# Kernel tuning notes

Measured on AMD Instinct MI355X. Metric: run time of the kernel, lower is better.

The kernel has to match this reference:

```python
import jax, jax.numpy as jnp
import numpy as np

B, N, NODE_DIM, HID_DIM = 64, 4096, 128, 128
D = NODE_DIM + HID_DIM  # concat of ndata['h'] and ndata['x']


def setup_inputs() -> dict:
    key = jax.random.key(0)
    k1, k2, k3, k4 = jax.random.split(key, 4)
    feats = jax.random.normal(k1, (B, N, D), dtype=jnp.float32)
    # per-graph node counts in [1, N] (split_batch asserts size != 0)
    node_counts = jax.random.randint(k2, (B,), 1, N + 1, dtype=jnp.int32)
    Wi = jax.random.normal(k3, (D, 1), dtype=jnp.float32) * 0.05   # project_i weight
    bi = jnp.zeros((1,), dtype=jnp.float32)
    Wj = jax.random.normal(k4, (D, HID_DIM), dtype=jnp.float32) * 0.05  # project_j weight
    bj = jnp.zeros((HID_DIM,), dtype=jnp.float32)
    return {"feats": feats, "node_counts": node_counts,
            "Wi": Wi, "bi": bi, "Wj": Wj, "bj": bj}


def reference(feats, node_counts, Wi, bi, Wj, bj):
    # mask: True at padded node slots (equivalent to zero-pad + sum==0 in split_batch)
    n = feats.shape[1]
    mask = jnp.arange(n)[None, :] >= node_counts[:, None]          # [B, N]
    feats = jnp.where(mask[..., None], 0.0, feats)                  # zero padding rows
    scores = feats @ Wi + bi                                        # [B, N, 1]
    scores = jnp.where(mask[..., None], -100000.0, scores)          # masked_fill
    h1 = jax.nn.softmax(scores, axis=1)                             # softmax over nodes
    h2 = feats @ Wj + bj                                            # [B, N, HID_DIM]
    return jnp.einsum('bni,bnj->bj', h1, h2)                        # [B, HID_DIM]
```

## Files before the change

### kernel.cpp

```cpp
#include <hip/hip_runtime.h>


#define NDIM 256
#define HID 128
#define NMAX 4096
#define ROWS_PER_BLK 160
#define NCHUNK 26
#define PSTRIDE 260
#define FLAG_MAGIC 0x5EED5EEDu

__global__ __launch_bounds__(512) void pool_fused(
    const float* __restrict__ feats, const int* __restrict__ counts,
    const float* __restrict__ Wi, const float* __restrict__ bi,
    const float* __restrict__ Wj, const float* __restrict__ bj,
    unsigned int* __restrict__ flags, float* __restrict__ part_g,
    float* __restrict__ out)
{
    const int b     = blockIdx.y;
    const int count = counts[b];
    const int tid   = threadIdx.x;
    const int nch   = (count + ROWS_PER_BLK - 1) / ROWS_PER_BLK;

    __shared__ float lds_acc[8][NDIM];
    __shared__ float lds_l[8];
    __shared__ float red[2][NDIM];
    __shared__ float redl[2];
    __shared__ float pooled[NDIM];
    __shared__ float tmp[4][HID];

    if (blockIdx.x < NCHUNK) {
        const int row0 = blockIdx.x * ROWS_PER_BLK;
        if (row0 >= count) return;
        const int row_end = min(row0 + ROWS_PER_BLK, count);

        const int lane = tid & 63;
        const int wv   = tid >> 6;
        const int g    = lane >> 4;
        const int q    = lane & 15;

        const float4* Wi4 = reinterpret_cast<const float4*>(Wi);
        const float4 wi0 = Wi4[q], wi1 = Wi4[16 + q], wi2 = Wi4[32 + q], wi3 = Wi4[48 + q];
        const float  fbi = bi[0];

        const float* fb = feats + (size_t)b * NMAX * NDIM;

        float4 a0 = {0,0,0,0}, a1 = {0,0,0,0}, a2 = {0,0,0,0}, a3 = {0,0,0,0};
        float lsum = 0.f;

        const int wbase = row0 + wv * 20;
        #pragma unroll
        for (int it = 0; it < 5; ++it) {
            const int r = wbase + it * 4 + g;
            const bool valid = (r < row_end);
            float4 f0 = {0,0,0,0}, f1 = {0,0,0,0}, f2 = {0,0,0,0}, f3 = {0,0,0,0};
            if (valid) {
                const float4* rp = reinterpret_cast<const float4*>(fb + (size_t)r * NDIM);
                f0 = rp[q]; f1 = rp[16 + q]; f2 = rp[32 + q]; f3 = rp[48 + q];
            }
            float sp = f0.x*wi0.x + f0.y*wi0.y + f0.z*wi0.z + f0.w*wi0.w
                     + f1.x*wi1.x + f1.y*wi1.y + f1.z*wi1.z + f1.w*wi1.w
                     + f2.x*wi2.x + f2.y*wi2.y + f2.z*wi2.z + f2.w*wi2.w
                     + f3.x*wi3.x + f3.y*wi3.y + f3.z*wi3.z + f3.w*wi3.w;
            sp += __shfl_xor(sp, 1, 64);
            sp += __shfl_xor(sp, 2, 64);
            sp += __shfl_xor(sp, 4, 64);
            sp += __shfl_xor(sp, 8, 64);
            const float w = valid ? __expf(sp + fbi) : 0.f;
            lsum += w;
            a0.x += w*f0.x; a0.y += w*f0.y; a0.z += w*f0.z; a0.w += w*f0.w;
            a1.x += w*f1.x; a1.y += w*f1.y; a1.z += w*f1.z; a1.w += w*f1.w;
            a2.x += w*f2.x; a2.y += w*f2.y; a2.z += w*f2.z; a2.w += w*f2.w;
            a3.x += w*f3.x; a3.y += w*f3.y; a3.z += w*f3.z; a3.w += w*f3.w;
        }

        #define COMB(x) x += __shfl_xor(x, 16, 64); x += __shfl_xor(x, 32, 64)
        COMB(a0.x); COMB(a0.y); COMB(a0.z); COMB(a0.w);
        COMB(a1.x); COMB(a1.y); COMB(a1.z); COMB(a1.w);
        COMB(a2.x); COMB(a2.y); COMB(a2.z); COMB(a2.w);
        COMB(a3.x); COMB(a3.y); COMB(a3.z); COMB(a3.w);
        COMB(lsum);
        #undef COMB

        if (g == 0) {
            float* dst = &lds_acc[wv][0];
            *reinterpret_cast<float4*>(&dst[q*4      ]) = a0;
            *reinterpret_cast<float4*>(&dst[q*4 +  64]) = a1;
            *reinterpret_cast<float4*>(&dst[q*4 + 128]) = a2;
            *reinterpret_cast<float4*>(&dst[q*4 + 192]) = a3;
            if (q == 0) lds_l[wv] = lsum;
        }
        __syncthreads();

        float* part = part_g + (size_t)(b * NCHUNK + blockIdx.x) * PSTRIDE;
        if (tid < NDIM) {
            float v = 0.f;
            #pragma unroll
            for (int k = 0; k < 8; ++k) v += lds_acc[k][tid];
            __hip_atomic_store(&part[tid], v, __ATOMIC_RELAXED,
                               __HIP_MEMORY_SCOPE_AGENT);
        } else if (tid == NDIM) {
            float v = 0.f;
            #pragma unroll
            for (int k = 0; k < 8; ++k) v += lds_l[k];
            __hip_atomic_store(&part[NDIM], v, __ATOMIC_RELAXED,
                               __HIP_MEMORY_SCOPE_AGENT);
        }
        __syncthreads();
        if (tid == 0)
            __hip_atomic_store(&flags[b * NCHUNK + blockIdx.x], FLAG_MAGIC,
                               __ATOMIC_RELAXED, __HIP_MEMORY_SCOPE_AGENT);
        return;
    }

    if (tid < 64) {
        for (int c = (int)tid; c < nch; c += 64)
            while (__hip_atomic_load(&flags[b * NCHUNK + c], __ATOMIC_RELAXED,
                                     __HIP_MEMORY_SCOPE_AGENT) != FLAG_MAGIC)
                __builtin_amdgcn_s_sleep(2);
    }
    __syncthreads();
    asm volatile("" ::: "memory");

    const int t    = tid & (NDIM - 1);
    const int half = tid >> 8;
    float acc = 0.f, l = 0.f;
    for (int c = half; c < nch; c += 2) {
        const float* p = part_g + (size_t)(b * NCHUNK + c) * PSTRIDE;
        acc += p[t];
        l   += p[NDIM];
    }
    red[half][t] = acc;
    if (t == 0) redl[half] = l;
    __syncthreads();
    if (tid < NDIM)
        pooled[tid] = (red[0][tid] + red[1][tid]) / (redl[0] + redl[1]);
    __syncthreads();

    const int j  = tid & (HID - 1);
    const int ks = (tid >> 7) * 64;
    float s = 0.f;
    #pragma unroll 16
    for (int k = 0; k < 64; ++k)
        s += pooled[ks + k] * Wj[(ks + k) * HID + j];
    tmp[tid >> 7][j] = s;
    __syncthreads();
    if (tid < HID)
        out[b * HID + tid] = tmp[0][tid] + tmp[1][tid] + tmp[2][tid]
                           + tmp[3][tid] + bj[tid];
}

extern "C" void kernel_launch(void* const* d_in, const int* in_sizes, int n_in,
                              void* d_out, int out_size, void* d_ws, size_t ws_size,
                              hipStream_t stream) {
    const float* feats  = (const float*)d_in[0];
    const int*   counts = (const int*)  d_in[1];
    const float* Wi     = (const float*)d_in[2];
    const float* bi     = (const float*)d_in[3];
    const float* Wj     = (const float*)d_in[4];
    const float* bj     = (const float*)d_in[5];
    float* out = (float*)d_out;

    const int B = in_sizes[1];

    unsigned int* flags  = (unsigned int*)d_ws;
    float*        part_g = (float*)((char*)d_ws + 16384);

    dim3 g1(NCHUNK + 1, B);
    pool_fused<<<g1, 512, 0, stream>>>(feats, counts, Wi, bi, Wj, bj,
                                       flags, part_g, out);
}
```

Before: 25.34 us.

## Replace spin-wait finisher block with atomic accumulation and last-block-done epilogue

```diff
diff --git a/kernel.cpp b/kernel.cpp
--- a/kernel.cpp
+++ b/kernel.cpp
@@ -6,14 +6,14 @@
 #define NMAX 4096
 #define ROWS_PER_BLK 160
 #define NCHUNK 26
-#define PSTRIDE 260
-#define FLAG_MAGIC 0x5EED5EEDu
+#define ASTRIDE 257
+#define ALOAD(p) __hip_atomic_load((p), __ATOMIC_RELAXED, __HIP_MEMORY_SCOPE_AGENT)
 
 __global__ __launch_bounds__(512) void pool_fused(
     const float* __restrict__ feats, const int* __restrict__ counts,
     const float* __restrict__ Wi, const float* __restrict__ bi,
     const float* __restrict__ Wj, const float* __restrict__ bj,
-    unsigned int* __restrict__ flags, float* __restrict__ part_g,
+    unsigned int* __restrict__ done, float* __restrict__ acc_g,
     float* __restrict__ out)
 {
     const int b     = blockIdx.y;
@@ -21,119 +21,101 @@
     const int tid   = threadIdx.x;
     const int nch   = (count + ROWS_PER_BLK - 1) / ROWS_PER_BLK;
 
+    const int row0 = blockIdx.x * ROWS_PER_BLK;
+    if (row0 >= count) return;
+    const int row_end = min(row0 + ROWS_PER_BLK, count);
+
     __shared__ float lds_acc[8][NDIM];
     __shared__ float lds_l[8];
-    __shared__ float red[2][NDIM];
-    __shared__ float redl[2];
     __shared__ float pooled[NDIM];
     __shared__ float tmp[4][HID];
+    __shared__ unsigned int s_old;
 
-    if (blockIdx.x < NCHUNK) {
-        const int row0 = blockIdx.x * ROWS_PER_BLK;
-        if (row0 >= count) return;
-        const int row_end = min(row0 + ROWS_PER_BLK, count);
+    const int lane = tid & 63;
+    const int wv   = tid >> 6;
+    const int g    = lane >> 4;
+    const int q    = lane & 15;
 
-        const int lane = tid & 63;
-        const int wv   = tid >> 6;
-        const int g    = lane >> 4;
-        const int q    = lane & 15;
+    const float4* Wi4 = reinterpret_cast<const float4*>(Wi);
+    const float4 wi0 = Wi4[q], wi1 = Wi4[16 + q], wi2 = Wi4[32 + q], wi3 = Wi4[48 + q];
+    const float  fbi = bi[0];
 
-        const float4* Wi4 = reinterpret_cast<const float4*>(Wi);
-        const float4 wi0 = Wi4[q], wi1 = Wi4[16 + q], wi2 = Wi4[32 + q], wi3 = Wi4[48 + q];
-        const float  fbi = bi[0];
+    const float* fb = feats + (size_t)b * NMAX * NDIM;
 
-        const float* fb = feats + (size_t)b * NMAX * NDIM;
+    float4 a0 = {0,0,0,0}, a1 = {0,0,0,0}, a2 = {0,0,0,0}, a3 = {0,0,0,0};
+    float lsum = 0.f;
 
-        float4 a0 = {0,0,0,0}, a1 = {0,0,0,0}, a2 = {0,0,0,0}, a3 = {0,0,0,0};
-        float lsum = 0.f;
-
-        const int wbase = row0 + wv * 20;
-        #pragma unroll
-        for (int it = 0; it < 5; ++it) {
-            const int r = wbase + it * 4 + g;
-            const bool valid = (r < row_end);
-            float4 f0 = {0,0,0,0}, f1 = {0,0,0,0}, f2 = {0,0,0,0}, f3 = {0,0,0,0};
-            if (valid) {
-                const float4* rp = reinterpret_cast<const float4*>(fb + (size_t)r * NDIM);
-                f0 = rp[q]; f1 = rp[16 + q]; f2 = rp[32 + q]; f3 = rp[48 + q];
-            }
-            float sp = f0.x*wi0.x + f0.y*wi0.y + f0.z*wi0.z + f0.w*wi0.w
-                     + f1.x*wi1.x + f1.y*wi1.y + f1.z*wi1.z + f1.w*wi1.w
-                     + f2.x*wi2.x + f2.y*wi2.y + f2.z*wi2.z + f2.w*wi2.w
-                     + f3.x*wi3.x + f3.y*wi3.y + f3.z*wi3.z + f3.w*wi3.w;
-            sp += __shfl_xor(sp, 1, 64);
-            sp += __shfl_xor(sp, 2, 64);
-            sp += __shfl_xor(sp, 4, 64);
-            sp += __shfl_xor(sp, 8, 64);
-            const float w = valid ? __expf(sp + fbi) : 0.f;
-            lsum += w;
-            a0.x += w*f0.x; a0.y += w*f0.y; a0.z += w*f0.z; a0.w += w*f0.w;
-            a1.x += w*f1.x; a1.y += w*f1.y; a1.z += w*f1.z; a1.w += w*f1.w;
-            a2.x += w*f2.x; a2.y += w*f2.y; a2.z += w*f2.z; a2.w += w*f2.w;
-            a3.x += w*f3.x; a3.y += w*f3.y; a3.z += w*f3.z; a3.w += w*f3.w;
+    const int wbase = row0 + wv * 20;
+    #pragma unroll
+    for (int it = 0; it < 5; ++it) {
+        const int r = wbase + it * 4 + g;
+        const bool valid = (r < row_end);
+        float4 f0 = {0,0,0,0}, f1 = {0,0,0,0}, f2 = {0,0,0,0}, f3 = {0,0,0,0};
+        if (valid) {
+            const float4* rp = reinterpret_cast<const float4*>(fb + (size_t)r * NDIM);
+            f0 = rp[q]; f1 = rp[16 + q]; f2 = rp[32 + q]; f3 = rp[48 + q];
         }
-
-        #define COMB(x) x += __shfl_xor(x, 16, 64); x += __shfl_xor(x, 32, 64)
-        COMB(a0.x); COMB(a0.y); COMB(a0.z); COMB(a0.w);
-        COMB(a1.x); COMB(a1.y); COMB(a1.z); COMB(a1.w);
-        COMB(a2.x); COMB(a2.y); COMB(a2.z); COMB(a2.w);
-        COMB(a3.x); COMB(a3.y); COMB(a3.z); COMB(a3.w);
-        COMB(lsum);
-        #undef COMB
-
-        if (g == 0) {
-            float* dst = &lds_acc[wv][0];
-            *reinterpret_cast<float4*>(&dst[q*4      ]) = a0;
-            *reinterpret_cast<float4*>(&dst[q*4 +  64]) = a1;
-            *reinterpret_cast<float4*>(&dst[q*4 + 128]) = a2;
-            *reinterpret_cast<float4*>(&dst[q*4 + 192]) = a3;
-            if (q == 0) lds_l[wv] = lsum;
-        }
-        __syncthreads();
-
-        float* part = part_g + (size_t)(b * NCHUNK + blockIdx.x) * PSTRIDE;
-        if (tid < NDIM) {
-            float v = 0.f;
-            #pragma unroll
-            for (int k = 0; k < 8; ++k) v += lds_acc[k][tid];
-            __hip_atomic_store(&part[tid], v, __ATOMIC_RELAXED,
-                               __HIP_MEMORY_SCOPE_AGENT);
-        } else if (tid == NDIM) {
-            float v = 0.f;
-            #pragma unroll
-            for (int k = 0; k < 8; ++k) v += lds_l[k];
-            __hip_atomic_store(&part[NDIM], v, __ATOMIC_RELAXED,
-                               __HIP_MEMORY_SCOPE_AGENT);
-        }
-        __syncthreads();
-        if (tid == 0)
-            __hip_atomic_store(&flags[b * NCHUNK + blockIdx.x], FLAG_MAGIC,
-                               __ATOMIC_RELAXED, __HIP_MEMORY_SCOPE_AGENT);
-        return;
+        float sp = f0.x*wi0.x + f0.y*wi0.y + f0.z*wi0.z + f0.w*wi0.w
+                 + f1.x*wi1.x + f1.y*wi1.y + f1.z*wi1.z + f1.w*wi1.w
+                 + f2.x*wi2.x + f2.y*wi2.y + f2.z*wi2.z + f2.w*wi2.w
+                 + f3.x*wi3.x + f3.y*wi3.y + f3.z*wi3.z + f3.w*wi3.w;
+        sp += __shfl_xor(sp, 1, 64);
+        sp += __shfl_xor(sp, 2, 64);
+        sp += __shfl_xor(sp, 4, 64);
+        sp += __shfl_xor(sp, 8, 64);
+        const float w = valid ? __expf(sp + fbi) : 0.f;
+        lsum += w;
+        a0.x += w*f0.x; a0.y += w*f0.y; a0.z += w*f0.z; a0.w += w*f0.w;
+        a1.x += w*f1.x; a1.y += w*f1.y; a1.z += w*f1.z; a1.w += w*f1.w;
+        a2.x += w*f2.x; a2.y += w*f2.y; a2.z += w*f2.z; a2.w += w*f2.w;
+        a3.x += w*f3.x; a3.y += w*f3.y; a3.z += w*f3.z; a3.w += w*f3.w;
     }
 
-    if (tid < 64) {
-        for (int c = (int)tid; c < nch; c += 64)
-            while (__hip_atomic_load(&flags[b * NCHUNK + c], __ATOMIC_RELAXED,
-                                     __HIP_MEMORY_SCOPE_AGENT) != FLAG_MAGIC)
-                __builtin_amdgcn_s_sleep(2);
+    #define COMB(x) x += __shfl_xor(x, 16, 64); x += __shfl_xor(x, 32, 64)
+    COMB(a0.x); COMB(a0.y); COMB(a0.z); COMB(a0.w);
+    COMB(a1.x); COMB(a1.y); COMB(a1.z); COMB(a1.w);
+    COMB(a2.x); COMB(a2.y); COMB(a2.z); COMB(a2.w);
+    COMB(a3.x); COMB(a3.y); COMB(a3.z); COMB(a3.w);
+    COMB(lsum);
+    #undef COMB
+
+    if (g == 0) {
+        float* dst = &lds_acc[wv][0];
+        *reinterpret_cast<float4*>(&dst[q*4      ]) = a0;
+        *reinterpret_cast<float4*>(&dst[q*4 +  64]) = a1;
+        *reinterpret_cast<float4*>(&dst[q*4 + 128]) = a2;
+        *reinterpret_cast<float4*>(&dst[q*4 + 192]) = a3;
+        if (q == 0) lds_l[wv] = lsum;
     }
     __syncthreads();
-    asm volatile("" ::: "memory");
 
-    const int t    = tid & (NDIM - 1);
-    const int half = tid >> 8;
-    float acc = 0.f, l = 0.f;
-    for (int c = half; c < nch; c += 2) {
-        const float* p = part_g + (size_t)(b * NCHUNK + c) * PSTRIDE;
-        acc += p[t];
-        l   += p[NDIM];
+    float* acc = acc_g + (size_t)b * ASTRIDE;
+    if (tid < NDIM) {
+        float v = 0.f;
+        #pragma unroll
+        for (int k = 0; k < 8; ++k) v += lds_acc[k][tid];
+        float old = atomicAdd(&acc[tid], v);
+        asm volatile("" :: "v"(old));
+    } else if (tid == NDIM) {
+        float lv = 0.f;
+        #pragma unroll
+        for (int k = 0; k < 8; ++k) lv += lds_l[k];
+        float old = atomicAdd(&acc[NDIM], lv);
+        asm volatile("" :: "v"(old));
     }
-    red[half][t] = acc;
-    if (t == 0) redl[half] = l;
     __syncthreads();
-    if (tid < NDIM)
-        pooled[tid] = (red[0][tid] + red[1][tid]) / (redl[0] + redl[1]);
+
+    if (tid == 0) s_old = atomicAdd(&done[b], 1u);
+    __syncthreads();
+    if (s_old != (unsigned int)(nch - 1)) return;
+
+    {
+        const float lv = ALOAD(&acc[NDIM]);
+        if (tid < NDIM) {
+            const float av = ALOAD(&acc[tid]);
+            pooled[tid] = av / lv;
+        }
+    }
     __syncthreads();
 
     const int j  = tid & (HID - 1);
@@ -162,10 +144,12 @@
 
     const int B = in_sizes[1];
 
-    unsigned int* flags  = (unsigned int*)d_ws;
-    float*        part_g = (float*)((char*)d_ws + 16384);
+    unsigned int* done  = (unsigned int*)d_ws;
+    float*        acc_g = (float*)((char*)d_ws + 256);
 
-    dim3 g1(NCHUNK + 1, B);
+    hipMemsetAsync(d_ws, 0, 256 + (size_t)B * ASTRIDE * sizeof(float), stream);
+
+    dim3 g1(NCHUNK, B);
     pool_fused<<<g1, 512, 0, stream>>>(feats, counts, Wi, bi, Wj, bj,
-                                       flags, part_g, out);
+                                       done, acc_g, out);
 }
```

Measured after the change: 33.84 us. +33.5%, slower.
